# Optimization experiments

Hardware: AMD Instinct MI355X
Metric: run time of the kernel (lower is better)

The kernel has to match this reference:

```python
import jax, jax.numpy as jnp
import numpy as np

ROPE_BASE = 10000.0
NUM_HEADS = 16
NUM_KV_HEADS = 4


def _rms_norm(x, eps):
    # F.rms_norm with no weight: x / sqrt(mean(x^2) + eps)
    return x * jax.lax.rsqrt(jnp.mean(x * x, axis=-1, keepdims=True) + eps)


def _apply_rope(x, cos, sin):
    h = x.shape[-1] // 2
    x1, x2 = x[..., :h], x[..., h:]
    return jnp.concatenate([x1 * cos + x2 * sin, -x1 * sin + x2 * cos], axis=-1)


def setup_inputs() -> dict:
    key = jax.random.key(0)
    ks = jax.random.split(key, 5)
    B, T, D = 2, 2048, 1024
    H, Hkv = NUM_HEADS, NUM_KV_HEADS
    hd = D // H
    kv_dim = Hkv * hd
    s_in = 1.0 / np.sqrt(D)
    return {
        "x": jax.random.normal(ks[0], (B, T, D), dtype=jnp.float32),
        "Wq": jax.random.normal(ks[1], (D, D), dtype=jnp.float32) * s_in,
        "Wk": jax.random.normal(ks[2], (kv_dim, D), dtype=jnp.float32) * s_in,
        "Wv": jax.random.normal(ks[3], (kv_dim, D), dtype=jnp.float32) * s_in,
        "Wproj": jax.random.normal(ks[4], (D, D), dtype=jnp.float32) * s_in,
        "q_gain": jnp.full((H,), 1.0, dtype=jnp.float32),
    }


def reference(x, Wq, Wk, Wv, Wproj, q_gain):
    B, T, D = x.shape
    H, Hkv = NUM_HEADS, NUM_KV_HEADS
    hd = D // H
    rep = H // Hkv
    eps = jnp.finfo(x.dtype).eps

    # QKV projections (F.linear: x @ W.T)
    q = jnp.einsum('btd,od->bto', x, Wq).reshape(B, T, H, hd).transpose(0, 2, 1, 3)
    k = jnp.einsum('btd,od->bto', x, Wk).reshape(B, T, Hkv, hd).transpose(0, 2, 1, 3)
    v = jnp.einsum('btd,od->bto', x, Wv).reshape(B, T, Hkv, hd).transpose(0, 2, 1, 3)

    q = _rms_norm(q, eps)
    k = _rms_norm(k, eps)

    # RoPE tables: [1, 1, T, hd/2]
    inv_freq = 1.0 / (ROPE_BASE ** (jnp.arange(0, hd, 2, dtype=jnp.float32) / hd))
    f = jnp.arange(T, dtype=jnp.float32)[:, None] * inv_freq[None, :]
    cos = jnp.cos(f)[None, None].astype(q.dtype)
    sin = jnp.sin(f)[None, None].astype(q.dtype)
    q = _apply_rope(q, cos, sin)
    k = _apply_rope(k, cos, sin)

    q = q * q_gain.astype(q.dtype)[None, :, None, None]

    # GQA without materializing repeated K/V: group q heads [Hkv, rep]
    qg = q.reshape(B, Hkv, rep, T, hd)
    scale = hd ** -0.5
    scores = jnp.einsum('bgrqd,bgkd->bgrqk', qg, k) * scale
    causal = jnp.tril(jnp.ones((T, T), dtype=bool))
    scores = jnp.where(causal, scores, -jnp.inf)
    att = jax.nn.softmax(scores.astype(jnp.float32), axis=-1).astype(q.dtype)
    y = jnp.einsum('bgrqk,bgkd->bgrqd', att, v)  # [B,Hkv,rep,T,hd]
    y = y.reshape(B, H, T, hd).transpose(0, 2, 1, 3).reshape(B, T, D)
    return jnp.einsum('btd,od->bto', y, Wproj)
```

## Files before the change

### kernel.cpp

```cpp
#include <hip/hip_runtime.h>
#include <cstdint>
#include <cstddef>

typedef __attribute__((ext_vector_type(8))) short short8;
typedef __attribute__((ext_vector_type(4))) float floatx4;
typedef __attribute__((ext_vector_type(4))) short short4v;
typedef unsigned short u16;
typedef unsigned int u32;

#define B_   2
#define T_   2048
#define D_   1024
#define H_   16
#define HKV_ 4
#define HD_  64
#define KV_  256
#define M_   4096
#define QS_  1536

#define NX   4194304
#define NWQ  1048576
#define NWK  262144
#define NWV  262144
#define NWP  1048576
#define NCAST (NX + NWQ + NWK + NWV + NWP)
#define CAST_BLOCKS (NCAST / 1024)
#define TAB_BLOCKS  256

__device__ __forceinline__ float b2f(u16 u) {
    union { u32 i; float f; } v; v.i = ((u32)u) << 16; return v.f;
}
__device__ __forceinline__ u16 f2b(float f) {
    union { float f; u32 i; } v; v.f = f;
    u32 r = v.i + 0x7FFF + ((v.i >> 16) & 1);
    return (u16)(r >> 16);
}
__device__ __forceinline__ u32 pack_hi(float a, float b) {
    union { float f; u32 u; } ua, ub; ua.f = a; ub.f = b;
    return (ua.u >> 16) | (ub.u & 0xFFFF0000u);
}

__device__ __forceinline__ void async16(const u16* g, u16* l) {
    __builtin_amdgcn_global_load_lds(
        (const __attribute__((address_space(1))) u32*)g,
        (__attribute__((address_space(3))) u32*)l, 16, 0, 0);
}

__global__ __launch_bounds__(256) void prep(const float* __restrict__ x,
                                            const float* __restrict__ wq,
                                            const float* __restrict__ wk,
                                            const float* __restrict__ wv,
                                            const float* __restrict__ wp,
                                            u16* __restrict__ dst,
                                            float2* __restrict__ tab) {
    int blk = blockIdx.x;
    if (blk < CAST_BLOCKS) {
        int i = blk * 1024 + threadIdx.x * 4;
        const float* src; int off;
        if      (i < NX)                  { src = x;  off = i; }
        else if (i < NX+NWQ)              { src = wq; off = i - NX; }
        else if (i < NX+NWQ+NWK)          { src = wk; off = i - (NX+NWQ); }
        else if (i < NX+NWQ+NWK+NWV)      { src = wv; off = i - (NX+NWQ+NWK); }
        else                              { src = wp; off = i - (NX+NWQ+NWK+NWV); }
        float4 v = *(const float4*)(src + off);
        short4v o;
        o.x = (short)f2b(v.x); o.y = (short)f2b(v.y);
        o.z = (short)f2b(v.z); o.w = (short)f2b(v.w);
        *(short4v*)(dst + i) = o;
    } else {
        int idx = (blk - CAST_BLOCKS) * 256 + threadIdx.x;
        int t = idx >> 5, i = idx & 31;
        float freq = exp2f(-(float)i * (13.287712379549449f / 32.0f));
        float ang = (float)t * freq;
        tab[idx] = make_float2(cosf(ang), sinf(ang));
    }
}

__global__ __launch_bounds__(256) void gemm_qkv(const u16* __restrict__ A,
                                                const u16* __restrict__ W,
                                                u16* __restrict__ C,
                                                u16* __restrict__ Vt,
                                                const float* __restrict__ gain,
                                                const float2* __restrict__ tab) {
    const int K = D_;
    __shared__ u16 As[128 * 32];
    __shared__ u16 Bs[128 * 32];
    const int t = threadIdx.x;
    const int wave = t >> 6, lane = t & 63;
    const int quad = lane >> 4, l16 = lane & 15;
    const int wm = (wave >> 1) * 64, wn = (wave & 1) * 64;
    const int m0 = blockIdx.y * 128, n0 = blockIdx.x * 128;

    floatx4 acc[4][4];
#pragma unroll
    for (int i = 0; i < 4; i++)
#pragma unroll
        for (int j = 0; j < 4; j++) acc[i][j] = (floatx4){0.f, 0.f, 0.f, 0.f};

    const int sr = t >> 2, sc = (t & 3) * 8;
    const u16* ga = A + (size_t)(m0 + sr) * K + sc;
    const u16* gb = W + (size_t)(n0 + sr) * K + sc;
    u16* lA = As + t * 8;
    u16* lB = Bs + t * 8;

    async16(ga, lA);
    async16(ga + (size_t)64 * K, lA + 64 * 32);
    async16(gb, lB);
    async16(gb + (size_t)64 * K, lB + 64 * 32);

    for (int kt = 0; kt < K; kt += 32) {
        __syncthreads();
        short8 af[4], bf[4];
#pragma unroll
        for (int mt = 0; mt < 4; mt++)
            af[mt] = *(const short8*)(As + (wm + mt * 16 + l16) * 32 + quad * 8);
#pragma unroll
        for (int nt = 0; nt < 4; nt++)
            bf[nt] = *(const short8*)(Bs + (wn + nt * 16 + l16) * 32 + quad * 8);
#pragma unroll
        for (int mt = 0; mt < 4; mt++)
#pragma unroll
            for (int nt = 0; nt < 4; nt++)
                acc[mt][nt] = __builtin_amdgcn_mfma_f32_16x16x32_bf16(
                    af[mt], bf[nt], acc[mt][nt], 0, 0, 0);
        __syncthreads();
        if (kt + 32 < K) {
            const u16* ga2 = ga + kt + 32;
            const u16* gb2 = gb + kt + 32;
            async16(ga2, lA);
            async16(ga2 + (size_t)64 * K, lA + 64 * 32);
            async16(gb2, lB);
            async16(gb2 + (size_t)64 * K, lB + 64 * 32);
        }
    }

    const int col0 = n0 + wn;
    if (col0 < 1280) {
        float gs = (col0 < 1024)
                 ? gain[col0 >> 6] * (0.125f * 1.4426950408889634f)
                 : 1.0f;
#pragma unroll
        for (int mt = 0; mt < 4; mt++)
#pragma unroll
            for (int r = 0; r < 4; r++) {
                int row = m0 + wm + mt * 16 + quad * 4 + r;
                int tt = row & (T_ - 1);
                float v0 = acc[mt][0][r], v1 = acc[mt][1][r];
                float v2 = acc[mt][2][r], v3 = acc[mt][3][r];
                float ss = v0 * v0 + v1 * v1 + v2 * v2 + v3 * v3;
                ss += __shfl_xor(ss, 1); ss += __shfl_xor(ss, 2);
                ss += __shfl_xor(ss, 4); ss += __shfl_xor(ss, 8);
                float inv = rsqrtf(ss * (1.0f / 64.0f) + 1.1920929e-7f);
                v0 *= inv; v1 *= inv; v2 *= inv; v3 *= inv;
                float2 cs0 = tab[tt * 32 + l16];
                float2 cs1 = tab[tt * 32 + 16 + l16];
                float o0 = (v0 * cs0.x + v2 * cs0.y) * gs;
                float o1 = (v1 * cs1.x + v3 * cs1.y) * gs;
                float o2 = (v2 * cs0.x - v0 * cs0.y) * gs;
                float o3 = (v3 * cs1.x - v1 * cs1.y) * gs;
                u16* cp = C + (size_t)row * QS_ + col0 + l16;
                cp[0]  = f2b(o0);
                cp[16] = f2b(o1);
                cp[32] = f2b(o2);
                cp[48] = f2b(o3);
            }
    } else {
        const int g = (col0 - 1280) >> 6;
#pragma unroll
        for (int mt = 0; mt < 4; mt++)
#pragma unroll
            for (int r = 0; r < 4; r++) {
                int row = m0 + wm + mt * 16 + quad * 4 + r;
                int tt = row & (T_ - 1);
                int bb = row >> 11;
#pragma unroll
                for (int nt = 0; nt < 4; nt++)
                    Vt[(size_t)((bb * 4 + g) * 64 + nt * 16 + l16) * T_ + tt] =
                        f2b(acc[mt][nt][r]);
            }
    }
}

template <typename OutT>
__global__ __launch_bounds__(256) void gemm128(const u16* __restrict__ A,
                                               const u16* __restrict__ W,
                                               OutT* __restrict__ C,
                                               int M, int N, int K, int ldc) {
    __shared__ u16 As[128 * 32];
    __shared__ u16 Bs[128 * 32];
    const int t = threadIdx.x;
    const int wave = t >> 6, lane = t & 63;
    const int quad = lane >> 4, l16 = lane & 15;
    const int wm = (wave >> 1) * 64, wn = (wave & 1) * 64;
    const int m0 = blockIdx.y * 128, n0 = blockIdx.x * 128;

    floatx4 acc[4][4];
#pragma unroll
    for (int i = 0; i < 4; i++)
#pragma unroll
        for (int j = 0; j < 4; j++) acc[i][j] = (floatx4){0.f, 0.f, 0.f, 0.f};

    const int sr = t >> 2, sc = (t & 3) * 8;
    const u16* ga = A + (size_t)(m0 + sr) * K + sc;
    const u16* gb = W + (size_t)(n0 + sr) * K + sc;
    u16* lA = As + t * 8;
    u16* lB = Bs + t * 8;

    async16(ga, lA);
    async16(ga + (size_t)64 * K, lA + 64 * 32);
    async16(gb, lB);
    async16(gb + (size_t)64 * K, lB + 64 * 32);

    for (int kt = 0; kt < K; kt += 32) {
        __syncthreads();
        short8 af[4], bf[4];
#pragma unroll
        for (int mt = 0; mt < 4; mt++)
            af[mt] = *(const short8*)(As + (wm + mt * 16 + l16) * 32 + quad * 8);
#pragma unroll
        for (int nt = 0; nt < 4; nt++)
            bf[nt] = *(const short8*)(Bs + (wn + nt * 16 + l16) * 32 + quad * 8);
#pragma unroll
        for (int mt = 0; mt < 4; mt++)
#pragma unroll
            for (int nt = 0; nt < 4; nt++)
                acc[mt][nt] = __builtin_amdgcn_mfma_f32_16x16x32_bf16(
                    af[mt], bf[nt], acc[mt][nt], 0, 0, 0);
        __syncthreads();
        if (kt + 32 < K) {
            const u16* ga2 = ga + kt + 32;
            const u16* gb2 = gb + kt + 32;
            async16(ga2, lA);
            async16(ga2 + (size_t)64 * K, lA + 64 * 32);
            async16(gb2, lB);
            async16(gb2 + (size_t)64 * K, lB + 64 * 32);
        }
    }

#pragma unroll
    for (int mt = 0; mt < 4; mt++)
#pragma unroll
        for (int nt = 0; nt < 4; nt++)
#pragma unroll
            for (int r = 0; r < 4; r++) {
                int row = m0 + wm + mt * 16 + quad * 4 + r;
                int col = n0 + wn + nt * 16 + l16;
                float val = acc[mt][nt][r];
                if constexpr (sizeof(OutT) == 4) C[(size_t)row * ldc + col] = val;
                else                             C[(size_t)row * ldc + col] = (OutT)f2b(val);
            }
}

__global__ __launch_bounds__(256) void flash(const u16* __restrict__ QKV,
                                             const u16* __restrict__ Vtr,
                                             u16* __restrict__ Y) {
    const int xp = blockIdx.x;
    const int h  = blockIdx.y;
    const int b  = blockIdx.z;
    const int g  = h >> 2;
    const int w    = threadIdx.x >> 6;
    const int lane = threadIdx.x & 63;
    const int quad = lane >> 4, l16 = lane & 15;

    __shared__ u16 Kt[64 * 64];
    __shared__ u16 Vs[64 * 64];
    __shared__ __align__(16) u16 P[4][2][16][72];

    const int mA = xp * 64 + w * 16;
    const int mB = (31 - xp) * 64 + w * 16;
    const int nA = xp + 1;
    const int nB = 32 - xp;

    const u16* qpA = QKV + (size_t)(b * T_ + mA + l16) * QS_ + h * HD_ + quad * 8;
    const u16* qpB = QKV + (size_t)(b * T_ + mB + l16) * QS_ + h * HD_ + quad * 8;
    short8 aqA0 = *(const short8*)(qpA);
    short8 aqA1 = *(const short8*)(qpA + 32);
    short8 aqB0 = *(const short8*)(qpB);
    short8 aqB1 = *(const short8*)(qpB + 32);

    short8 ones;
#pragma unroll
    for (int i = 0; i < 8; i++) ones[i] = (short)0x3F80;

    floatx4 accA[4], accB[4];
#pragma unroll
    for (int i = 0; i < 4; i++) {
        accA[i] = (floatx4){0.f, 0.f, 0.f, 0.f};
        accB[i] = (floatx4){0.f, 0.f, 0.f, 0.f};
    }
    floatx4 lAcc = (floatx4){0.f, 0.f, 0.f, 0.f};
    floatx4 lBcc = (floatx4){0.f, 0.f, 0.f, 0.f};

    const int srow = w * 16 + (lane >> 3);
    const int sseg = (lane & 7) ^ ((lane >> 3) & 7);
    const u16* kg = QKV + (size_t)(b * T_ + srow) * QS_ + D_ + g * 64 + sseg * 8;
    const u16* vg = Vtr + (size_t)((b * 4 + g) * 64 + srow) * T_ + sseg * 8;
    u16* klds = Kt + w * 1024 + lane * 8;
    u16* vlds = Vs + w * 1024 + lane * 8;

    const int sw0 = (quad ^ (l16 & 7)) * 8;
    const int sw1 = ((4 + quad) ^ (l16 & 7)) * 8;

    async16(kg, klds);
    async16(kg + (size_t)8 * QS_, klds + 512);
    async16(vg, vlds);
    async16(vg + (size_t)8 * T_, vlds + 512);

    for (int tk = 0; tk < nB; tk++) {
        const bool dual = (tk < nA);
        __syncthreads();

        floatx4 SB[4], SA[4];
#pragma unroll
        for (int nt = 0; nt < 4; nt++) {
            const u16* kr = Kt + (nt * 16 + l16) * 64;
            short8 kf0 = *(const short8*)(kr + sw0);
            short8 kf1 = *(const short8*)(kr + sw1);
            SB[nt] = (floatx4){0.f, 0.f, 0.f, 0.f};
            SB[nt] = __builtin_amdgcn_mfma_f32_16x16x32_bf16(kf0, aqB0, SB[nt], 0, 0, 0);
            SB[nt] = __builtin_amdgcn_mfma_f32_16x16x32_bf16(kf1, aqB1, SB[nt], 0, 0, 0);
            if (dual) {
                SA[nt] = (floatx4){0.f, 0.f, 0.f, 0.f};
                SA[nt] = __builtin_amdgcn_mfma_f32_16x16x32_bf16(kf0, aqA0, SA[nt], 0, 0, 0);
                SA[nt] = __builtin_amdgcn_mfma_f32_16x16x32_bf16(kf1, aqA1, SA[nt], 0, 0, 0);
            }
        }
        short8 vf[4][2];
#pragma unroll
        for (int dd = 0; dd < 4; dd++) {
            const u16* vr = Vs + (dd * 16 + l16) * 64;
            vf[dd][0] = *(const short8*)(vr + sw0);
            vf[dd][1] = *(const short8*)(vr + sw1);
        }
        __syncthreads();
        if (tk + 1 < nB) {
            kg += (size_t)64 * QS_;
            vg += 64;
            async16(kg, klds);
            async16(kg + (size_t)8 * QS_, klds + 512);
            async16(vg, vlds);
            async16(vg + (size_t)8 * T_, vlds + 512);
        }

        const bool maskB = (tk == nB - 1);
        const int qB = mB + l16;
#pragma unroll
        for (int nt = 0; nt < 4; nt++) {
            float p[4];
#pragma unroll
            for (int r = 0; r < 4; r++) {
                float e = __builtin_amdgcn_exp2f(SB[nt][r]);
                if (maskB) {
                    int key = tk * 64 + nt * 16 + quad * 4 + r;
                    e = (key <= qB) ? e : 0.f;
                }
                p[r] = e;
            }
            uint2 pw; pw.x = pack_hi(p[0], p[1]); pw.y = pack_hi(p[2], p[3]);
            *(uint2*)&P[w][1][l16][nt * 16 + quad * 4] = pw;
        }
        short8 pfB0 = *(const short8*)&P[w][1][l16][quad * 8];
        short8 pfB1 = *(const short8*)&P[w][1][l16][quad * 8 + 32];
#pragma unroll
        for (int dd = 0; dd < 4; dd++) {
            accB[dd] = __builtin_amdgcn_mfma_f32_16x16x32_bf16(pfB0, vf[dd][0], accB[dd], 0, 0, 0);
            accB[dd] = __builtin_amdgcn_mfma_f32_16x16x32_bf16(pfB1, vf[dd][1], accB[dd], 0, 0, 0);
        }
        lBcc = __builtin_amdgcn_mfma_f32_16x16x32_bf16(pfB0, ones, lBcc, 0, 0, 0);
        lBcc = __builtin_amdgcn_mfma_f32_16x16x32_bf16(pfB1, ones, lBcc, 0, 0, 0);

        if (dual) {
            const bool maskA = (tk == nA - 1);
            const int qA = mA + l16;
#pragma unroll
            for (int nt = 0; nt < 4; nt++) {
                float p[4];
#pragma unroll
                for (int r = 0; r < 4; r++) {
                    float e = __builtin_amdgcn_exp2f(SA[nt][r]);
                    if (maskA) {
                        int key = tk * 64 + nt * 16 + quad * 4 + r;
                        e = (key <= qA) ? e : 0.f;
                    }
                    p[r] = e;
                }
                uint2 pw; pw.x = pack_hi(p[0], p[1]); pw.y = pack_hi(p[2], p[3]);
                *(uint2*)&P[w][0][l16][nt * 16 + quad * 4] = pw;
            }
            short8 pfA0 = *(const short8*)&P[w][0][l16][quad * 8];
            short8 pfA1 = *(const short8*)&P[w][0][l16][quad * 8 + 32];
#pragma unroll
            for (int dd = 0; dd < 4; dd++) {
                accA[dd] = __builtin_amdgcn_mfma_f32_16x16x32_bf16(pfA0, vf[dd][0], accA[dd], 0, 0, 0);
                accA[dd] = __builtin_amdgcn_mfma_f32_16x16x32_bf16(pfA1, vf[dd][1], accA[dd], 0, 0, 0);
            }
            lAcc = __builtin_amdgcn_mfma_f32_16x16x32_bf16(pfA0, ones, lAcc, 0, 0, 0);
            lAcc = __builtin_amdgcn_mfma_f32_16x16x32_bf16(pfA1, ones, lAcc, 0, 0, 0);
        }
    }

#pragma unroll
    for (int r = 0; r < 4; r++) {
        float invA = 1.0f / lAcc[r];
        float invB = 1.0f / lBcc[r];
        int rowA = mA + quad * 4 + r;
        int rowB = mB + quad * 4 + r;
        u16* ypA = Y + (size_t)(b * T_ + rowA) * D_ + h * HD_ + l16;
        u16* ypB = Y + (size_t)(b * T_ + rowB) * D_ + h * HD_ + l16;
#pragma unroll
        for (int dd = 0; dd < 4; dd++) {
            ypA[dd * 16] = f2b(accA[dd][r] * invA);
            ypB[dd * 16] = f2b(accB[dd][r] * invB);
        }
    }
}

extern "C" void kernel_launch(void* const* d_in, const int* in_sizes, int n_in,
                              void* d_out, int out_size, void* d_ws, size_t ws_size,
                              hipStream_t stream) {
    const float* x    = (const float*)d_in[0];
    const float* Wq   = (const float*)d_in[1];
    const float* Wk   = (const float*)d_in[2];
    const float* Wv   = (const float*)d_in[3];
    const float* Wp   = (const float*)d_in[4];
    const float* gain = (const float*)d_in[5];
    float* out = (float*)d_out;

    u16* xb   = (u16*)d_ws;
    u16* Wcat = xb + (size_t)NX;
    u16* Wpb  = Wcat + (size_t)(NWQ + NWK + NWV);
    u16* QKV  = Wpb + (size_t)NWP;
    u16* Vt   = QKV + (size_t)M_ * QS_;
    u16* Y    = Vt + (size_t)M_ * KV_;
    float2* tab = (float2*)(Y + (size_t)M_ * D_);

    prep<<<CAST_BLOCKS + TAB_BLOCKS, 256, 0, stream>>>(x, Wq, Wk, Wv, Wp, xb, tab);

    gemm_qkv<<<dim3(QS_ / 128, M_ / 128), 256, 0, stream>>>(xb, Wcat, QKV, Vt,
                                                            gain, tab);

    flash<<<dim3(16, H_, B_), 256, 0, stream>>>(QKV, Vt, Y);

    gemm128<float><<<dim3(D_ / 128, M_ / 128), 256, 0, stream>>>(Y, Wpb, out,
                                                                 M_, D_, D_, D_);
}
```

Measured before the change: 179.6 us.

## Double-buffer LDS tiles in GEMM and flash-attention loops

Converts the shared-memory A/B tiles in both GEMM kernels and the K/V tiles in the flash-attention kernel to two-stage ping-pong buffers. The next tile's async global-to-LDS load is now issued right after the single barrier and before computing on the current buffer, so load latency overlaps with the MFMA work. This drops one __syncthreads per iteration. In exchange it doubles LDS use for these tiles, which may reduce occupancy. Correctness relies on the barrier also waiting for the outstanding async loads.

```diff
diff --git a/kernel.cpp b/kernel.cpp
--- a/kernel.cpp
+++ b/kernel.cpp
@@ -83,8 +83,8 @@
                                                 const float* __restrict__ gain,
                                                 const float2* __restrict__ tab) {
     const int K = D_;
-    __shared__ u16 As[128 * 32];
-    __shared__ u16 Bs[128 * 32];
+    __shared__ u16 As[2][128 * 32];
+    __shared__ u16 Bs[2][128 * 32];
     const int t = threadIdx.x;
     const int wave = t >> 6, lane = t & 63;
     const int quad = lane >> 4, l16 = lane & 15;
@@ -100,38 +100,39 @@
     const int sr = t >> 2, sc = (t & 3) * 8;
     const u16* ga = A + (size_t)(m0 + sr) * K + sc;
     const u16* gb = W + (size_t)(n0 + sr) * K + sc;
-    u16* lA = As + t * 8;
-    u16* lB = Bs + t * 8;
-
-    async16(ga, lA);
-    async16(ga + (size_t)64 * K, lA + 64 * 32);
-    async16(gb, lB);
-    async16(gb + (size_t)64 * K, lB + 64 * 32);
-
+
+    async16(ga, As[0] + t * 8);
+    async16(ga + (size_t)64 * K, As[0] + t * 8 + 64 * 32);
+    async16(gb, Bs[0] + t * 8);
+    async16(gb + (size_t)64 * K, Bs[0] + t * 8 + 64 * 32);
+
+    int cur = 0;
     for (int kt = 0; kt < K; kt += 32) {
-        __syncthreads();
-        short8 af[4], bf[4];
-#pragma unroll
-        for (int mt = 0; mt < 4; mt++)
-            af[mt] = *(const short8*)(As + (wm + mt * 16 + l16) * 32 + quad * 8);
-#pragma unroll
-        for (int nt = 0; nt < 4; nt++)
-            bf[nt] = *(const short8*)(Bs + (wn + nt * 16 + l16) * 32 + quad * 8);
-#pragma unroll
-        for (int mt = 0; mt < 4; mt++)
-#pragma unroll
-            for (int nt = 0; nt < 4; nt++)
-                acc[mt][nt] = __builtin_amdgcn_mfma_f32_16x16x32_bf16(
-                    af[mt], bf[nt], acc[mt][nt], 0, 0, 0);
         __syncthreads();
         if (kt + 32 < K) {
             const u16* ga2 = ga + kt + 32;
             const u16* gb2 = gb + kt + 32;
+            u16* lA = As[cur ^ 1] + t * 8;
+            u16* lB = Bs[cur ^ 1] + t * 8;
             async16(ga2, lA);
             async16(ga2 + (size_t)64 * K, lA + 64 * 32);
             async16(gb2, lB);
             async16(gb2 + (size_t)64 * K, lB + 64 * 32);
         }
+        short8 af[4], bf[4];
+#pragma unroll
+        for (int mt = 0; mt < 4; mt++)
+            af[mt] = *(const short8*)(As[cur] + (wm + mt * 16 + l16) * 32 + quad * 8);
+#pragma unroll
+        for (int nt = 0; nt < 4; nt++)
+            bf[nt] = *(const short8*)(Bs[cur] + (wn + nt * 16 + l16) * 32 + quad * 8);
+#pragma unroll
+        for (int mt = 0; mt < 4; mt++)
+#pragma unroll
+            for (int nt = 0; nt < 4; nt++)
+                acc[mt][nt] = __builtin_amdgcn_mfma_f32_16x16x32_bf16(
+                    af[mt], bf[nt], acc[mt][nt], 0, 0, 0);
+        cur ^= 1;
     }
 
     const int col0 = n0 + wn;
@@ -186,8 +187,8 @@
                                                const u16* __restrict__ W,
                                                OutT* __restrict__ C,
                                                int M, int N, int K, int ldc) {
-    __shared__ u16 As[128 * 32];
-    __shared__ u16 Bs[128 * 32];
+    __shared__ u16 As[2][128 * 32];
+    __shared__ u16 Bs[2][128 * 32];
     const int t = threadIdx.x;
     const int wave = t >> 6, lane = t & 63;
     const int quad = lane >> 4, l16 = lane & 15;
@@ -203,38 +204,39 @@
     const int sr = t >> 2, sc = (t & 3) * 8;
     const u16* ga = A + (size_t)(m0 + sr) * K + sc;
     const u16* gb = W + (size_t)(n0 + sr) * K + sc;
-    u16* lA = As + t * 8;
-    u16* lB = Bs + t * 8;
-
-    async16(ga, lA);
-    async16(ga + (size_t)64 * K, lA + 64 * 32);
-    async16(gb, lB);
-    async16(gb + (size_t)64 * K, lB + 64 * 32);
-
+
+    async16(ga, As[0] + t * 8);
+    async16(ga + (size_t)64 * K, As[0] + t * 8 + 64 * 32);
+    async16(gb, Bs[0] + t * 8);
+    async16(gb + (size_t)64 * K, Bs[0] + t * 8 + 64 * 32);
+
+    int cur = 0;
     for (int kt = 0; kt < K; kt += 32) {
-        __syncthreads();
-        short8 af[4], bf[4];
-#pragma unroll
-        for (int mt = 0; mt < 4; mt++)
-            af[mt] = *(const short8*)(As + (wm + mt * 16 + l16) * 32 + quad * 8);
-#pragma unroll
-        for (int nt = 0; nt < 4; nt++)
-            bf[nt] = *(const short8*)(Bs + (wn + nt * 16 + l16) * 32 + quad * 8);
-#pragma unroll
-        for (int mt = 0; mt < 4; mt++)
-#pragma unroll
-            for (int nt = 0; nt < 4; nt++)
-                acc[mt][nt] = __builtin_amdgcn_mfma_f32_16x16x32_bf16(
-                    af[mt], bf[nt], acc[mt][nt], 0, 0, 0);
         __syncthreads();
         if (kt + 32 < K) {
             const u16* ga2 = ga + kt + 32;
             const u16* gb2 = gb + kt + 32;
+            u16* lA = As[cur ^ 1] + t * 8;
+            u16* lB = Bs[cur ^ 1] + t * 8;
             async16(ga2, lA);
             async16(ga2 + (size_t)64 * K, lA + 64 * 32);
             async16(gb2, lB);
             async16(gb2 + (size_t)64 * K, lB + 64 * 32);
         }
+        short8 af[4], bf[4];
+#pragma unroll
+        for (int mt = 0; mt < 4; mt++)
+            af[mt] = *(const short8*)(As[cur] + (wm + mt * 16 + l16) * 32 + quad * 8);
+#pragma unroll
+        for (int nt = 0; nt < 4; nt++)
+            bf[nt] = *(const short8*)(Bs[cur] + (wn + nt * 16 + l16) * 32 + quad * 8);
+#pragma unroll
+        for (int mt = 0; mt < 4; mt++)
+#pragma unroll
+            for (int nt = 0; nt < 4; nt++)
+                acc[mt][nt] = __builtin_amdgcn_mfma_f32_16x16x32_bf16(
+                    af[mt], bf[nt], acc[mt][nt], 0, 0, 0);
+        cur ^= 1;
     }
 
 #pragma unroll
@@ -262,8 +264,8 @@
     const int lane = threadIdx.x & 63;
     const int quad = lane >> 4, l16 = lane & 15;
 
-    __shared__ u16 Kt[64 * 64];
-    __shared__ u16 Vs[64 * 64];
+    __shared__ u16 Kt[2][64 * 64];
+    __shared__ u16 Vs[2][64 * 64];
     __shared__ __align__(16) u16 P[4][2][16][72];
 
     const int mA = xp * 64 + w * 16;
@@ -295,25 +297,34 @@
     const int sseg = (lane & 7) ^ ((lane >> 3) & 7);
     const u16* kg = QKV + (size_t)(b * T_ + srow) * QS_ + D_ + g * 64 + sseg * 8;
     const u16* vg = Vtr + (size_t)((b * 4 + g) * 64 + srow) * T_ + sseg * 8;
-    u16* klds = Kt + w * 1024 + lane * 8;
-    u16* vlds = Vs + w * 1024 + lane * 8;
 
     const int sw0 = (quad ^ (l16 & 7)) * 8;
     const int sw1 = ((4 + quad) ^ (l16 & 7)) * 8;
 
-    async16(kg, klds);
-    async16(kg + (size_t)8 * QS_, klds + 512);
-    async16(vg, vlds);
-    async16(vg + (size_t)8 * T_, vlds + 512);
-
+    async16(kg, Kt[0] + w * 1024 + lane * 8);
+    async16(kg + (size_t)8 * QS_, Kt[0] + w * 1024 + lane * 8 + 512);
+    async16(vg, Vs[0] + w * 1024 + lane * 8);
+    async16(vg + (size_t)8 * T_, Vs[0] + w * 1024 + lane * 8 + 512);
+
+    int cur = 0;
     for (int tk = 0; tk < nB; tk++) {
         const bool dual = (tk < nA);
         __syncthreads();
+        if (tk + 1 < nB) {
+            kg += (size_t)64 * QS_;
+            vg += 64;
+            u16* klds = Kt[cur ^ 1] + w * 1024 + lane * 8;
+            u16* vlds = Vs[cur ^ 1] + w * 1024 + lane * 8;
+            async16(kg, klds);
+            async16(kg + (size_t)8 * QS_, klds + 512);
+            async16(vg, vlds);
+            async16(vg + (size_t)8 * T_, vlds + 512);
+        }
 
         floatx4 SB[4], SA[4];
 #pragma unroll
         for (int nt = 0; nt < 4; nt++) {
-            const u16* kr = Kt + (nt * 16 + l16) * 64;
+            const u16* kr = Kt[cur] + (nt * 16 + l16) * 64;
             short8 kf0 = *(const short8*)(kr + sw0);
             short8 kf1 = *(const short8*)(kr + sw1);
             SB[nt] = (floatx4){0.f, 0.f, 0.f, 0.f};
@@ -328,18 +339,9 @@
         short8 vf[4][2];
 #pragma unroll
         for (int dd = 0; dd < 4; dd++) {
-            const u16* vr = Vs + (dd * 16 + l16) * 64;
+            const u16* vr = Vs[cur] + (dd * 16 + l16) * 64;
             vf[dd][0] = *(const short8*)(vr + sw0);
             vf[dd][1] = *(const short8*)(vr + sw1);
-        }
-        __syncthreads();
-        if (tk + 1 < nB) {
-            kg += (size_t)64 * QS_;
-            vg += 64;
-            async16(kg, klds);
-            async16(kg + (size_t)8 * QS_, klds + 512);
-            async16(vg, vlds);
-            async16(vg + (size_t)8 * T_, vlds + 512);
         }
 
         const bool maskB = (tk == nB - 1);
@@ -397,6 +399,7 @@
             lAcc = __builtin_amdgcn_mfma_f32_16x16x32_bf16(pfA0, ones, lAcc, 0, 0, 0);
             lAcc = __builtin_amdgcn_mfma_f32_16x16x32_bf16(pfA1, ones, lAcc, 0, 0, 0);
         }
+        cur ^= 1;
     }
 
 #pragma unroll
```

New measurement: 182.1 us. About the same (+1.4%).
